# Kernel tuning notes

Measured on AMD Instinct MI355X. Metric: run time of the kernel, lower is better.

Reference implementation:

```python
import jax, jax.numpy as jnp
import numpy as np

N = 500_000            # nodes
E = 16_000_000         # used edges (var edges); E_total = 2*E
EPS = 1e-5             # BatchNorm eps
SQRT_C = np.sqrt(2.0).astype(np.float32)  # out_channels=2


def setup_inputs() -> dict:
    key = jax.random.key(0)
    ks = jax.random.split(key, 20)
    w = lambda k, s: (jax.random.normal(k, s, jnp.float32) * 0.5)
    d = {}
    d["x"] = jax.random.normal(ks[0], (N, 2), jnp.float32)
    d["edge_index"] = jax.random.randint(ks[1], (2, 2 * E), 0, N, jnp.int32)
    d["edge_attr"] = jax.random.normal(ks[2], (2 * E, 2), jnp.float32)
    d["mask"] = (jax.random.uniform(ks[3], (N,)) < 0.5).astype(jnp.float32)
    # TransformerConv(2,2,edge_dim=2,heads=1) params
    d["Wq"], d["bq"] = w(ks[4], (2, 2)), w(ks[5], (2,))
    d["Wk"], d["bk"] = w(ks[6], (2, 2)), w(ks[7], (2,))
    d["Wv"], d["bv"] = w(ks[8], (2, 2)), w(ks[9], (2,))
    d["We"] = w(ks[10], (2, 2))               # lin_edge, bias=False
    d["Wskip"], d["bskip"] = w(ks[11], (2, 2)), w(ks[12], (2,))
    # BatchNorm(2) affine params
    d["gamma"], d["beta"] = jnp.ones((2,), jnp.float32), jnp.zeros((2,), jnp.float32)
    # final Linear(2,1)
    d["Wf"], d["bf"] = w(ks[13], (1, 2)), w(ks[14], (1,))
    return d


def _transformer_conv(x, src, dst, ea, Wq, bq, Wk, bk, Wv, bv, We, Wskip, bskip):
    # PyG TransformerConv, heads=1, concat=True, root_weight=True, beta=False
    q = x @ Wq.T + bq                       # [N,2]
    k = x @ Wk.T + bk                       # [N,2]
    v = x @ Wv.T + bv                       # [N,2]
    e = ea @ We.T                           # [E,2]
    k_j = k[src] + e                        # [E,2]
    alpha = jnp.sum(q[dst] * k_j, axis=1) / SQRT_C  # [E]
    # segment softmax over destination nodes
    m = jax.ops.segment_max(alpha, dst, num_segments=N)          # -inf for empty
    m = jnp.where(jnp.isfinite(m), m, 0.0)
    a = jnp.exp(alpha - m[dst])
    s = jax.ops.segment_sum(a, dst, num_segments=N)
    wgt = a / jnp.where(s[dst] > 0, s[dst], 1.0)                 # [E]
    msg = (v[src] + e) * wgt[:, None]                            # [E,2]
    out = jax.ops.segment_sum(msg, dst, num_segments=N)          # [N,2]
    return out + x @ Wskip.T + bskip


def _neighbor_max(x, src, dst, ea_clause):
    # vectorized form of the per-node Python loop (scatter-max)
    s = jnp.sum(x[src] * ea_clause, axis=1)                      # [E]
    seg = jax.ops.segment_max(s, dst, num_segments=N)            # [N]
    deg = jax.ops.segment_sum(jnp.ones_like(s), dst, num_segments=N)
    has = deg > 0
    mx = jnp.where(has, seg, 0.0)
    stacked = jnp.stack([mx, 1.0 - mx], axis=1)                  # [N,2]
    return jnp.where(has[:, None], stacked, x)


def reference(x, edge_index, edge_attr, mask, Wq, bq, Wk, bk, Wv, bv, We,
              Wskip, bskip, gamma, beta, Wf, bf):
    ei = edge_index[:, 1::2]        # var_index = odd columns
    ea = edge_attr[1::2]            # var edge attrs
    ea_clause = edge_attr[0::2]     # clause edge attrs
    src, dst = ei[0], ei[1]
    h = _transformer_conv(x, src, dst, ea, Wq, bq, Wk, bk, Wv, bv, We, Wskip, bskip)
    # BatchNorm1d, training-mode batch statistics (biased var)
    mu = jnp.mean(h, axis=0)
    var = jnp.mean((h - mu) ** 2, axis=0)
    h = (h - mu) / jnp.sqrt(var + EPS) * gamma + beta
    # softmax over node dim (dim=0)
    h = jax.nn.softmax(h, axis=0)
    h = _neighbor_max(h, src, dst, ea_clause)
    # iterations=1 -> extra loop body does not execute
    out = jnp.squeeze(h @ Wf.T + bf)       # [N]
    return out * mask
```

## Files before the change

kernel.cpp:

```cpp
#include <hip/hip_runtime.h>
#include <hip/hip_fp16.h>

#define NNODES 500000
#define NEDGES 16000000
#define NBLK 1024
#define EPB (NEDGES / NBLK)
#define BSH 11
#define BSZ 2048
#define NBKT 245
#define BDIM 256
#define CHUNK 2048
#define KPC (CHUNK / 256)
#define CTH 1024

typedef unsigned long long u64;
typedef unsigned int u32;
typedef unsigned short u16;
typedef float vf4 __attribute__((ext_vector_type(4)));


__device__ __forceinline__ u32 fmap_ord(float x) {
    u32 u = __float_as_uint(x);
    return (u & 0x80000000u) ? ~u : (u | 0x80000000u);
}
__device__ __forceinline__ float funmap_ord(u32 u) {
    u32 bits = (u & 0x80000000u) ? (u ^ 0x80000000u) : ~u;
    return __uint_as_float(bits);
}

__device__ __forceinline__ float4 ntload4(const float4* p) {
    vf4 v = __builtin_nontemporal_load((const vf4*)p);
    return make_float4(v.x, v.y, v.z, v.w);
}

__device__ __forceinline__ void block_reduce_atomic4(float v0, float v1, float v2, float v3,
                                                     float* dst) {
    for (int off = 32; off > 0; off >>= 1) {
        v0 += __shfl_down(v0, off, 64);
        v1 += __shfl_down(v1, off, 64);
        v2 += __shfl_down(v2, off, 64);
        v3 += __shfl_down(v3, off, 64);
    }
    __shared__ float red[4][4];
    int lane = threadIdx.x & 63, wid = threadIdx.x >> 6;
    if (lane == 0) { red[wid][0] = v0; red[wid][1] = v1; red[wid][2] = v2; red[wid][3] = v3; }
    __syncthreads();
    if (threadIdx.x < 4) {
        float t = red[0][threadIdx.x] + red[1][threadIdx.x] + red[2][threadIdx.x] + red[3][threadIdx.x];
        unsafeAtomicAdd(&dst[threadIdx.x], t);
    }
}

__device__ __forceinline__ void block_reduce_atomic4_w16(float v0, float v1, float v2, float v3,
                                                         float* dst) {
    for (int off = 32; off > 0; off >>= 1) {
        v0 += __shfl_down(v0, off, 64);
        v1 += __shfl_down(v1, off, 64);
        v2 += __shfl_down(v2, off, 64);
        v3 += __shfl_down(v3, off, 64);
    }
    __shared__ float red[16][4];
    int lane = threadIdx.x & 63, wid = threadIdx.x >> 6;
    if (lane == 0) { red[wid][0] = v0; red[wid][1] = v1; red[wid][2] = v2; red[wid][3] = v3; }
    __syncthreads();
    if (threadIdx.x < 4) {
        float t = 0.f;
        #pragma unroll
        for (int w = 0; w < 16; ++w) t += red[w][threadIdx.x];
        unsafeAtomicAdd(&dst[threadIdx.x], t);
    }
}


__global__ __launch_bounds__(64) void k_zero_accum(float* accum) {
    if (threadIdx.x < 16) accum[threadIdx.x] = 0.f;
}

__global__ __launch_bounds__(256) void k_node_prep(
    const float* __restrict__ x,
    const float* __restrict__ Wq, const float* __restrict__ bq,
    const float* __restrict__ Wk, const float* __restrict__ bk,
    const float* __restrict__ Wv, const float* __restrict__ bv,
    float2* __restrict__ q, uint2* __restrict__ kvh) {
    int i = blockIdx.x * blockDim.x + threadIdx.x;
    if (i >= NNODES) return;
    float2 xv = ((const float2*)x)[i];
    float q0 = fmaf(Wq[0], xv.x, fmaf(Wq[1], xv.y, bq[0]));
    float q1 = fmaf(Wq[2], xv.x, fmaf(Wq[3], xv.y, bq[1]));
    float k0 = fmaf(Wk[0], xv.x, fmaf(Wk[1], xv.y, bk[0]));
    float k1 = fmaf(Wk[2], xv.x, fmaf(Wk[3], xv.y, bk[1]));
    float v0 = fmaf(Wv[0], xv.x, fmaf(Wv[1], xv.y, bv[0]));
    float v1 = fmaf(Wv[2], xv.x, fmaf(Wv[3], xv.y, bv[1]));
    q[i] = make_float2(q0, q1);
    __half2 hk = __floats2half2_rn(k0, k1);
    __half2 hv = __floats2half2_rn(v0, v1);
    kvh[i] = make_uint2(*(u32*)&hk, *(u32*)&hv);
}

__global__ void k_ln_final(const float* __restrict__ gamma, const float* __restrict__ beta,
                           float* __restrict__ accum) {
    float n = (float)NNODES;
    float mu0 = accum[0] / n, mu1 = accum[1] / n;
    float var0 = accum[2] / n - mu0 * mu0;
    float var1 = accum[3] / n - mu1 * mu1;
    float sc0 = gamma[0] * rsqrtf(var0 + 1e-5f);
    float sc1 = gamma[1] * rsqrtf(var1 + 1e-5f);
    accum[8] = sc0;
    accum[9] = sc1;
    accum[10] = beta[0] - mu0 * sc0;
    accum[11] = beta[1] - mu1 * sc1;
}

__global__ __launch_bounds__(256) void k_softmax(
    const float2* __restrict__ h, float2* __restrict__ pp, float* __restrict__ accum) {
    int i = blockIdx.x * blockDim.x + threadIdx.x;
    float p0 = 0.f, p1 = 0.f;
    if (i < NNODES) {
        float sc0 = accum[8], sc1 = accum[9], sh0 = accum[10], sh1 = accum[11];
        float2 hv = h[i];
        p0 = __expf(fmaf(hv.x, sc0, sh0));
        p1 = __expf(fmaf(hv.y, sc1, sh1));
        pp[i] = make_float2(p0, p1);
    }
    block_reduce_atomic4(p0, p1, 0.f, 0.f, accum + 4);
}

__global__ void k_sm_final(float* __restrict__ accum) {
    accum[12] = 1.f / accum[4];
    accum[13] = 1.f / accum[5];
}


__global__ __launch_bounds__(256) void k_hist(const int2* __restrict__ dst2, u32* __restrict__ M) {
    __shared__ u32 hist[BDIM];
    if (threadIdx.x < BDIM) hist[threadIdx.x] = 0u;
    __syncthreads();
    int beg = blockIdx.x * EPB, end = beg + EPB;
    #pragma unroll 4
    for (int e = beg + threadIdx.x; e < end; e += 256)
        atomicAdd(&hist[dst2[e].y >> BSH], 1u);
    __syncthreads();
    u32* row = M + (size_t)blockIdx.x * BDIM;
    if (threadIdx.x < BDIM) row[threadIdx.x] = hist[threadIdx.x];
}

__global__ __launch_bounds__(256) void k_bucket_prefix(u32* __restrict__ M, u32* __restrict__ bucketTotal) {
    __shared__ u32 col[NBLK];
    int b = blockIdx.x;
    for (int j = threadIdx.x; j < NBLK; j += 256) col[j] = M[(size_t)j * BDIM + b];
    __syncthreads();
    if (threadIdx.x == 0) {
        u32 run = 0;
        for (int j = 0; j < NBLK; ++j) { u32 c = col[j]; col[j] = run; run += c; }
        bucketTotal[b] = run;
    }
    __syncthreads();
    for (int j = threadIdx.x; j < NBLK; j += 256) M[(size_t)j * BDIM + b] = col[j];
}

__global__ __launch_bounds__(256) void k_scan_serial(const u32* __restrict__ bucketTotal,
                                                     u32* __restrict__ bucketBase) {
    __shared__ u32 t[BDIM];
    __shared__ u32 o[BDIM + 1];
    if (threadIdx.x < BDIM) t[threadIdx.x] = bucketTotal[threadIdx.x];
    __syncthreads();
    if (threadIdx.x == 0) {
        u32 run = 0;
        for (int j = 0; j < BDIM; ++j) { o[j] = run; run += t[j]; }
        o[BDIM] = run;
    }
    __syncthreads();
    for (int j = threadIdx.x; j < BDIM + 1; j += 256) bucketBase[j] = o[j];
}


__global__ __launch_bounds__(256) void k_scatter_stg(
    const int2* __restrict__ src2, const int2* __restrict__ dst2,
    const float4* __restrict__ ea4, const float* __restrict__ We,
    const u32* __restrict__ M, const u32* __restrict__ bucketBase,
    float4* __restrict__ R) {
    __shared__ u32 hist[BDIM];
    __shared__ u32 lbase[BDIM];
    __shared__ u32 gcur[BDIM];
    __shared__ u32 wsum[4];
    __shared__ float4 buf[CHUNK];
    __shared__ u16 bkt[CHUNK];

    const u32* row = M + (size_t)blockIdx.x * BDIM;
    if (threadIdx.x < BDIM) gcur[threadIdx.x] = row[threadIdx.x] + bucketBase[threadIdx.x];
    float we00 = We[0], we01 = We[1], we10 = We[2], we11 = We[3];
    int beg = blockIdx.x * EPB;
    int lane = threadIdx.x & 63, wid = threadIdx.x >> 6;

    for (int c0 = 0; c0 < EPB; c0 += CHUNK) {
        int cn = min(CHUNK, EPB - c0);
        if (threadIdx.x < BDIM) hist[threadIdx.x] = 0u;
        __syncthreads();

        float4 recs[KPC]; u32 bks[KPC]; u32 rnk[KPC]; bool val[KPC];
        #pragma unroll
        for (int k = 0; k < KPC; ++k) {
            int tt = k * 256 + threadIdx.x;
            val[k] = tt < cn;
            if (val[k]) {
                int e = beg + c0 + tt;
                int si = src2[e].y;
                int di = dst2[e].y;
                float4 eav = ea4[e];
                float e0 = fmaf(we00, eav.z, we01 * eav.w);
                float e1 = fmaf(we10, eav.z, we11 * eav.w);
                __half2 hc = __floats2half2_rn(eav.x, eav.y);
                u32 b = (u32)di >> BSH;
                u32 idx = (u32)si | ((u32)(di & (BSZ - 1)) << 19);
                recs[k] = make_float4(__uint_as_float(idx), e0, e1,
                                      __uint_as_float(*(u32*)&hc));
                bks[k] = b;
                rnk[k] = atomicAdd(&hist[b], 1u);
            }
        }
        __syncthreads();

        u32 s = hist[threadIdx.x];
        u32 inc = s;
        #pragma unroll
        for (int d = 1; d < 64; d <<= 1) {
            u32 v = __shfl_up(inc, d, 64);
            if (lane >= d) inc += v;
        }
        if (lane == 63) wsum[wid] = inc;
        __syncthreads();
        u32 woff = 0;
        for (int w = 0; w < wid; ++w) woff += wsum[w];
        lbase[threadIdx.x] = woff + inc - s;
        __syncthreads();

        #pragma unroll
        for (int k = 0; k < KPC; ++k) {
            if (val[k]) {
                u32 p = lbase[bks[k]] + rnk[k];
                buf[p] = recs[k];
                bkt[p] = (u16)bks[k];
            }
        }
        __syncthreads();

        for (int j = threadIdx.x; j < cn; j += 256) {
            u32 b = bkt[j];
            R[(size_t)gcur[b] + (u32)j - lbase[b]] = buf[j];
        }
        __syncthreads();

        if (threadIdx.x < BDIM) gcur[threadIdx.x] += hist[threadIdx.x];
        __syncthreads();
    }
}

__global__ __launch_bounds__(CTH) void k_attn16(
    const float4* __restrict__ R,
    const u32* __restrict__ bucketBase, const u32* __restrict__ bucketTotal,
    const uint2* __restrict__ kvh, const float2* __restrict__ qp,
    const float* __restrict__ x,
    const float* __restrict__ Wskip, const float* __restrict__ bskip,
    float2* __restrict__ h, float* __restrict__ accum) {
    __shared__ float sA[BSZ], m0A[BSZ], m1A[BSZ];
    __shared__ float2 qT[BSZ];
    int b = blockIdx.x, base = b << BSH;
    for (int j = threadIdx.x; j < BSZ; j += CTH) {
        sA[j] = 0.f; m0A[j] = 0.f; m1A[j] = 0.f;
        int i = base + j;
        qT[j] = (i < NNODES) ? qp[i] : make_float2(0.f, 0.f);
    }
    __syncthreads();
    int beg = bucketBase[b], end = beg + bucketTotal[b];
    int idx = beg + threadIdx.x;
    for (; idx + 3 * CTH < end; idx += 4 * CTH) {
        float4 r[4];
        #pragma unroll
        for (int u = 0; u < 4; ++u) r[u] = ntload4(&R[idx + u * CTH]);
        int li[4]; uint2 kvv[4];
        #pragma unroll
        for (int u = 0; u < 4; ++u) {
            u32 rec = __float_as_uint(r[u].x);
            li[u] = rec >> 19;
            kvv[u] = kvh[rec & 0x7FFFFu];
        }
        #pragma unroll
        for (int u = 0; u < 4; ++u) {
            float2 kf = __half22float2(*(__half2*)&kvv[u].x);
            float2 vf = __half22float2(*(__half2*)&kvv[u].y);
            float2 qv = qT[li[u]];
            float alpha = fmaf(qv.x, kf.x + r[u].y, qv.y * (kf.y + r[u].z)) * 0.70710678118654752f;
            float a = __expf(alpha);
            atomicAdd(&sA[li[u]], a);
            atomicAdd(&m0A[li[u]], a * (vf.x + r[u].y));
            atomicAdd(&m1A[li[u]], a * (vf.y + r[u].z));
        }
    }
    for (; idx < end; idx += CTH) {
        float4 r = ntload4(&R[idx]);
        u32 rec = __float_as_uint(r.x);
        int li = rec >> 19;
        uint2 kvv = kvh[rec & 0x7FFFFu];
        float2 kf = __half22float2(*(__half2*)&kvv.x);
        float2 vf = __half22float2(*(__half2*)&kvv.y);
        float2 qv = qT[li];
        float alpha = fmaf(qv.x, kf.x + r.y, qv.y * (kf.y + r.z)) * 0.70710678118654752f;
        float a = __expf(alpha);
        atomicAdd(&sA[li], a);
        atomicAdd(&m0A[li], a * (vf.x + r.y));
        atomicAdd(&m1A[li], a * (vf.y + r.z));
    }
    __syncthreads();
    float r0 = 0.f, r1 = 0.f, r2 = 0.f, r3 = 0.f;
    float w00 = Wskip[0], w01 = Wskip[1], w10 = Wskip[2], w11 = Wskip[3];
    float c0 = bskip[0], c1 = bskip[1];
    for (int j = threadIdx.x; j < BSZ; j += CTH) {
        int i = base + j;
        if (i < NNODES) {
            float2 xv = ((const float2*)x)[i];
            float s = sA[j];
            float inv = s > 0.f ? 1.f / s : 0.f;
            float h0 = fmaf(m0A[j], inv, fmaf(w00, xv.x, fmaf(w01, xv.y, c0)));
            float h1 = fmaf(m1A[j], inv, fmaf(w10, xv.x, fmaf(w11, xv.y, c1)));
            h[i] = make_float2(h0, h1);
            r0 += h0; r1 += h1; r2 += h0 * h0; r3 += h1 * h1;
        }
    }
    block_reduce_atomic4_w16(r0, r1, r2, r3, accum);
}

__global__ __launch_bounds__(CTH) void k_nmax16(
    const float4* __restrict__ R,
    const u32* __restrict__ bucketBase, const u32* __restrict__ bucketTotal,
    const float2* __restrict__ pp, const float* __restrict__ accum,
    const float* __restrict__ Wf, const float* __restrict__ bf,
    const float* __restrict__ mask, float* __restrict__ out) {
    __shared__ u32 mxA[BSZ];
    __shared__ float maskT[BSZ];
    int b = blockIdx.x, base = b << BSH;
    for (int j = threadIdx.x; j < BSZ; j += CTH) {
        mxA[j] = 0u;
        int i = base + j;
        maskT[j] = (i < NNODES) ? mask[i] : 0.f;
    }
    __syncthreads();
    float inv0 = accum[12], inv1 = accum[13];
    int beg = bucketBase[b], end = beg + bucketTotal[b];
    int idx = beg + threadIdx.x;
    for (; idx + 3 * CTH < end; idx += 4 * CTH) {
        float4 r[4];
        #pragma unroll
        for (int u = 0; u < 4; ++u) r[u] = ntload4(&R[idx + u * CTH]);
        #pragma unroll
        for (int u = 0; u < 4; ++u) {
            u32 rec = __float_as_uint(r[u].x);
            int li = rec >> 19;
            if (maskT[li] == 0.f) continue;
            int si = rec & 0x7FFFFu;
            u32 hcbits = __float_as_uint(r[u].w);
            __half2 hc = *(__half2*)&hcbits;
            float2 cf = __half22float2(hc);
            float2 pv = pp[si];
            float sE = fmaf(pv.x * inv0, cf.x, pv.y * inv1 * cf.y);
            atomicMax(&mxA[li], fmap_ord(sE));
        }
    }
    for (; idx < end; idx += CTH) {
        float4 r = ntload4(&R[idx]);
        u32 rec = __float_as_uint(r.x);
        int li = rec >> 19;
        if (maskT[li] == 0.f) continue;
        int si = rec & 0x7FFFFu;
        u32 hcbits = __float_as_uint(r.w);
        __half2 hc = *(__half2*)&hcbits;
        float2 cf = __half22float2(hc);
        float2 pv = pp[si];
        float sE = fmaf(pv.x * inv0, cf.x, pv.y * inv1 * cf.y);
        atomicMax(&mxA[li], fmap_ord(sE));
    }
    __syncthreads();
    float wf0 = Wf[0], wf1 = Wf[1], bb = bf[0];
    for (int j = threadIdx.x; j < BSZ; j += CTH) {
        int i = base + j;
        if (i >= NNODES) continue;
        u32 m = mxA[j];
        float h0, h1;
        if (m != 0u) { float v = funmap_ord(m); h0 = v; h1 = 1.f - v; }
        else { float2 pv = pp[i]; h0 = pv.x * inv0; h1 = pv.y * inv1; }
        out[i] = fmaf(wf0, h0, fmaf(wf1, h1, bb)) * maskT[j];
    }
}


__global__ __launch_bounds__(256) void k_init_f(float* s, float* msg, u32* mxb, float* accum) {
    int i = blockIdx.x * blockDim.x + threadIdx.x;
    if (i < NNODES) { s[i] = 0.f; mxb[i] = 0u; }
    if (i < 2 * NNODES) msg[i] = 0.f;
    if (i < 16) accum[i] = 0.f;
}

__global__ __launch_bounds__(256) void k_node_prep_f(
    const float* __restrict__ x,
    const float* __restrict__ Wq, const float* __restrict__ bq,
    const float* __restrict__ Wk, const float* __restrict__ bk,
    const float* __restrict__ Wv, const float* __restrict__ bv,
    float2* __restrict__ q, float4* __restrict__ kv) {
    int i = blockIdx.x * blockDim.x + threadIdx.x;
    if (i >= NNODES) return;
    float2 xv = ((const float2*)x)[i];
    float q0 = fmaf(Wq[0], xv.x, fmaf(Wq[1], xv.y, bq[0]));
    float q1 = fmaf(Wq[2], xv.x, fmaf(Wq[3], xv.y, bq[1]));
    float k0 = fmaf(Wk[0], xv.x, fmaf(Wk[1], xv.y, bk[0]));
    float k1 = fmaf(Wk[2], xv.x, fmaf(Wk[3], xv.y, bk[1]));
    float v0 = fmaf(Wv[0], xv.x, fmaf(Wv[1], xv.y, bv[0]));
    float v1 = fmaf(Wv[2], xv.x, fmaf(Wv[3], xv.y, bv[1]));
    q[i] = make_float2(q0, q1);
    kv[i] = make_float4(k0, k1, v0, v1);
}

__global__ __launch_bounds__(256) void k_edge_attn_f(
    const int* __restrict__ ei, const float* __restrict__ ea,
    const float* __restrict__ We,
    const float2* __restrict__ q, const float4* __restrict__ kv,
    float* __restrict__ s, float* __restrict__ msg) {
    int e = blockIdx.x * blockDim.x + threadIdx.x;
    if (e >= NEDGES) return;
    float we00 = We[0], we01 = We[1], we10 = We[2], we11 = We[3];
    int si = ((const int2*)ei)[e].y;
    int di = ((const int2*)(ei + 2 * NEDGES))[e].y;
    float2 eav = ((const float2*)ea)[2 * e + 1];
    float4 kvv = kv[si];
    float2 qv = q[di];
    float e0 = fmaf(we00, eav.x, we01 * eav.y);
    float e1 = fmaf(we10, eav.x, we11 * eav.y);
    float alpha = fmaf(qv.x, kvv.x + e0, qv.y * (kvv.y + e1)) * 0.70710678118654752f;
    float a = __expf(alpha);
    unsafeAtomicAdd(&s[di], a);
    unsafeAtomicAdd(&msg[2 * di], a * (kvv.z + e0));
    unsafeAtomicAdd(&msg[2 * di + 1], a * (kvv.w + e1));
}

__global__ __launch_bounds__(256) void k_node_h_f(
    const float* __restrict__ x,
    const float* __restrict__ Wskip, const float* __restrict__ bskip,
    const float* __restrict__ s, float* __restrict__ msg, float* __restrict__ accum) {
    int i = blockIdx.x * blockDim.x + threadIdx.x;
    float h0 = 0.f, h1 = 0.f;
    if (i < NNODES) {
        float2 xv = ((const float2*)x)[i];
        float sk0 = fmaf(Wskip[0], xv.x, fmaf(Wskip[1], xv.y, bskip[0]));
        float sk1 = fmaf(Wskip[2], xv.x, fmaf(Wskip[3], xv.y, bskip[1]));
        float sv = s[i];
        float inv = sv > 0.f ? 1.f / sv : 0.f;
        h0 = fmaf(msg[2 * i], inv, sk0);
        h1 = fmaf(msg[2 * i + 1], inv, sk1);
        msg[2 * i] = h0;
        msg[2 * i + 1] = h1;
    }
    block_reduce_atomic4(h0, h1, h0 * h0, h1 * h1, accum);
}

__global__ __launch_bounds__(256) void k_edge_nmax_f(
    const int* __restrict__ ei, const float* __restrict__ ea,
    const float2* __restrict__ pp, const float* __restrict__ accum,
    u32* __restrict__ mxb) {
    int e = blockIdx.x * blockDim.x + threadIdx.x;
    if (e >= NEDGES) return;
    float inv0 = accum[12], inv1 = accum[13];
    int si = ((const int2*)ei)[e].y;
    int di = ((const int2*)(ei + 2 * NEDGES))[e].y;
    float2 c = ((const float2*)ea)[2 * e];
    float2 pv = pp[si];
    float sE = fmaf(pv.x * inv0, c.x, pv.y * inv1 * c.y);
    atomicMax(&mxb[di], fmap_ord(sE));
}

__global__ __launch_bounds__(256) void k_final_f(
    const u32* __restrict__ mxb, const float2* __restrict__ pp,
    const float* __restrict__ accum,
    const float* __restrict__ Wf, const float* __restrict__ bf,
    const float* __restrict__ mask, float* __restrict__ out) {
    int i = blockIdx.x * blockDim.x + threadIdx.x;
    if (i >= NNODES) return;
    u32 m = mxb[i];
    float h0, h1;
    if (m != 0u) {
        float v = funmap_ord(m);
        h0 = v;
        h1 = 1.f - v;
    } else {
        float2 pv = pp[i];
        h0 = pv.x * accum[12];
        h1 = pv.y * accum[13];
    }
    out[i] = fmaf(Wf[0], h0, fmaf(Wf[1], h1, bf[0])) * mask[i];
}


extern "C" void kernel_launch(void* const* d_in, const int* in_sizes, int n_in,
                              void* d_out, int out_size, void* d_ws, size_t ws_size,
                              hipStream_t stream) {
    const float* x     = (const float*)d_in[0];
    const int*   ei    = (const int*)d_in[1];
    const float* ea    = (const float*)d_in[2];
    const float* mask  = (const float*)d_in[3];
    const float* Wq    = (const float*)d_in[4];
    const float* bq    = (const float*)d_in[5];
    const float* Wk    = (const float*)d_in[6];
    const float* bk    = (const float*)d_in[7];
    const float* Wv    = (const float*)d_in[8];
    const float* bv    = (const float*)d_in[9];
    const float* We    = (const float*)d_in[10];
    const float* Wskip = (const float*)d_in[11];
    const float* bskip = (const float*)d_in[12];
    const float* gamma = (const float*)d_in[13];
    const float* beta  = (const float*)d_in[14];
    const float* Wf    = (const float*)d_in[15];
    const float* bf    = (const float*)d_in[16];
    float* out = (float*)d_out;

    const size_t N = NNODES;
    const size_t E = NEDGES;
    const int B = 256;
    const int gridN = (NNODES + B - 1) / B;

    const int2*   src2 = (const int2*)ei;
    const int2*   dst2 = (const int2*)(ei + 2 * NEDGES);
    const float4* ea4  = (const float4*)ea;

    size_t need16 = 8 * N
                  + 16 * E
                  + 8 * N
                  + 8 * N
                  + 8 * N
                  + 4 * (size_t)NBLK * BDIM
                  + 4 * BDIM
                  + 4 * (BDIM + 16)
                  + 64;

    if (ws_size >= need16) {
        char* base = (char*)d_ws;
        uint2*  kvh = (uint2*)base;                 base += 8 * N;
        float4* R  = (float4*)base;                 base += 16 * E;
        float2* q  = (float2*)base;                 base += 8 * N;
        float2* h  = (float2*)base;                 base += 8 * N;
        float2* p  = (float2*)base;                 base += 8 * N;
        u32*    M  = (u32*)base;                    base += 4 * (size_t)NBLK * BDIM;
        u32*    bT = (u32*)base;                    base += 4 * BDIM;
        u32*    bB = (u32*)base;                    base += 4 * (BDIM + 16);
        float*  accum = (float*)base;

        k_zero_accum<<<1, 64, 0, stream>>>(accum);
        k_node_prep<<<gridN, B, 0, stream>>>(x, Wq, bq, Wk, bk, Wv, bv, q, kvh);
        k_hist<<<NBLK, B, 0, stream>>>(dst2, M);
        k_bucket_prefix<<<BDIM, B, 0, stream>>>(M, bT);
        k_scan_serial<<<1, B, 0, stream>>>(bT, bB);
        k_scatter_stg<<<NBLK, B, 0, stream>>>(src2, dst2, ea4, We, M, bB, R);
        k_attn16<<<NBKT, CTH, 0, stream>>>(R, bB, bT, kvh, q, x, Wskip, bskip, h, accum);
        k_ln_final<<<1, 1, 0, stream>>>(gamma, beta, accum);
        k_softmax<<<gridN, B, 0, stream>>>(h, p, accum);
        k_sm_final<<<1, 1, 0, stream>>>(accum);
        k_nmax16<<<NBKT, CTH, 0, stream>>>(R, bB, bT, p, accum, Wf, bf, mask, out);
    } else {
        float*  q   = (float*)d_ws;
        float*  kvf = q + 2 * N;
        float*  s   = kvf + 4 * N;
        float*  msg = s + N;
        u32*    mxb = (u32*)(msg + 2 * N);
        float*  accum = (float*)(mxb + N);
        int grid2N = (int)((2 * N + B - 1) / B);
        int gridE  = (NEDGES + B - 1) / B;

        k_init_f<<<grid2N, B, 0, stream>>>(s, msg, mxb, accum);
        k_node_prep_f<<<gridN, B, 0, stream>>>(x, Wq, bq, Wk, bk, Wv, bv, (float2*)q, (float4*)kvf);
        k_edge_attn_f<<<gridE, B, 0, stream>>>(ei, ea, We, (const float2*)q, (const float4*)kvf, s, msg);
        k_node_h_f<<<gridN, B, 0, stream>>>(x, Wskip, bskip, s, msg, accum);
        k_ln_final<<<1, 1, 0, stream>>>(gamma, beta, accum);
        k_softmax<<<gridN, B, 0, stream>>>((const float2*)msg, (float2*)q, accum);
        k_sm_final<<<1, 1, 0, stream>>>(accum);
        k_edge_nmax_f<<<gridE, B, 0, stream>>>(ei, ea, (const float2*)q, accum, mxb);
        k_final_f<<<gridN, B, 0, stream>>>(mxb, (const float2*)q, accum, Wf, bf, mask, out);
    }
}
```

Measured before the change: 649.4 us.

## Split each dst bucket across two blocks with partial buffers and combine kernels

The attention and neighbor-max bucket kernels now launch two blocks per destination bucket, each handling half of the bucket's edges and writing partial sums or maxima to global buffers. New per-node kernels (k_node_h, k_final) merge the two halves and do the epilogue (skip connection, BN stats, final linear and mask). The aim is to fill more CUs, since there are only 245 buckets on a 256-CU device. The cost is extra global partial-buffer traffic, two more kernel launches, and twice the shared-memory init per bucket.

Result: slower. 693.4 us (+6.8%).

```diff
diff --git a/kernel.cpp b/kernel.cpp
--- a/kernel.cpp
+++ b/kernel.cpp
@@ -12,6 +12,7 @@
 #define CHUNK 2048
 #define KPC (CHUNK / 256)
 #define CTH 1024
+#define NP ((size_t)NBKT * BSZ)
 
 typedef unsigned long long u64;
 typedef unsigned int u32;
@@ -47,26 +48,6 @@
     __syncthreads();
     if (threadIdx.x < 4) {
         float t = red[0][threadIdx.x] + red[1][threadIdx.x] + red[2][threadIdx.x] + red[3][threadIdx.x];
-        unsafeAtomicAdd(&dst[threadIdx.x], t);
-    }
-}
-
-__device__ __forceinline__ void block_reduce_atomic4_w16(float v0, float v1, float v2, float v3,
-                                                         float* dst) {
-    for (int off = 32; off > 0; off >>= 1) {
-        v0 += __shfl_down(v0, off, 64);
-        v1 += __shfl_down(v1, off, 64);
-        v2 += __shfl_down(v2, off, 64);
-        v3 += __shfl_down(v3, off, 64);
-    }
-    __shared__ float red[16][4];
-    int lane = threadIdx.x & 63, wid = threadIdx.x >> 6;
-    if (lane == 0) { red[wid][0] = v0; red[wid][1] = v1; red[wid][2] = v2; red[wid][3] = v3; }
-    __syncthreads();
-    if (threadIdx.x < 4) {
-        float t = 0.f;
-        #pragma unroll
-        for (int w = 0; w < 16; ++w) t += red[w][threadIdx.x];
         unsafeAtomicAdd(&dst[threadIdx.x], t);
     }
 }
@@ -259,19 +240,23 @@
     const float4* __restrict__ R,
     const u32* __restrict__ bucketBase, const u32* __restrict__ bucketTotal,
     const uint2* __restrict__ kvh, const float2* __restrict__ qp,
-    const float* __restrict__ x,
-    const float* __restrict__ Wskip, const float* __restrict__ bskip,
-    float2* __restrict__ h, float* __restrict__ accum) {
+    float* __restrict__ pS, float* __restrict__ pM0, float* __restrict__ pM1) {
     __shared__ float sA[BSZ], m0A[BSZ], m1A[BSZ];
     __shared__ float2 qT[BSZ];
-    int b = blockIdx.x, base = b << BSH;
+    int blk = blockIdx.x;
+    int b = blk >> 1, half = blk & 1;
+    int base = b << BSH;
     for (int j = threadIdx.x; j < BSZ; j += CTH) {
         sA[j] = 0.f; m0A[j] = 0.f; m1A[j] = 0.f;
         int i = base + j;
         qT[j] = (i < NNODES) ? qp[i] : make_float2(0.f, 0.f);
     }
     __syncthreads();
-    int beg = bucketBase[b], end = beg + bucketTotal[b];
+    int len = bucketTotal[b];
+    int hlen = (len + 1) >> 1;
+    int beg = (int)bucketBase[b] + (half ? hlen : 0);
+    int cnt = half ? (len - hlen) : hlen;
+    int end = beg + cnt;
     int idx = beg + threadIdx.x;
     for (; idx + 3 * CTH < end; idx += 4 * CTH) {
         float4 r[4];
@@ -311,33 +296,46 @@
         atomicAdd(&m1A[li], a * (vf.y + r.z));
     }
     __syncthreads();
-    float r0 = 0.f, r1 = 0.f, r2 = 0.f, r3 = 0.f;
-    float w00 = Wskip[0], w01 = Wskip[1], w10 = Wskip[2], w11 = Wskip[3];
-    float c0 = bskip[0], c1 = bskip[1];
+    size_t off = (size_t)half * NP + (size_t)b * BSZ;
     for (int j = threadIdx.x; j < BSZ; j += CTH) {
-        int i = base + j;
-        if (i < NNODES) {
-            float2 xv = ((const float2*)x)[i];
-            float s = sA[j];
-            float inv = s > 0.f ? 1.f / s : 0.f;
-            float h0 = fmaf(m0A[j], inv, fmaf(w00, xv.x, fmaf(w01, xv.y, c0)));
-            float h1 = fmaf(m1A[j], inv, fmaf(w10, xv.x, fmaf(w11, xv.y, c1)));
-            h[i] = make_float2(h0, h1);
-            r0 += h0; r1 += h1; r2 += h0 * h0; r3 += h1 * h1;
-        }
-    }
-    block_reduce_atomic4_w16(r0, r1, r2, r3, accum);
+        pS[off + j]  = sA[j];
+        pM0[off + j] = m0A[j];
+        pM1[off + j] = m1A[j];
+    }
+}
+
+__global__ __launch_bounds__(256) void k_node_h(
+    const float* __restrict__ x,
+    const float* __restrict__ Wskip, const float* __restrict__ bskip,
+    const float* __restrict__ pS, const float* __restrict__ pM0, const float* __restrict__ pM1,
+    float2* __restrict__ h, float* __restrict__ accum) {
+    int i = blockIdx.x * blockDim.x + threadIdx.x;
+    float h0 = 0.f, h1 = 0.f;
+    if (i < NNODES) {
+        float s  = pS[i]  + pS[i + NP];
+        float m0 = pM0[i] + pM0[i + NP];
+        float m1 = pM1[i] + pM1[i + NP];
+        float2 xv = ((const float2*)x)[i];
+        float sk0 = fmaf(Wskip[0], xv.x, fmaf(Wskip[1], xv.y, bskip[0]));
+        float sk1 = fmaf(Wskip[2], xv.x, fmaf(Wskip[3], xv.y, bskip[1]));
+        float inv = s > 0.f ? 1.f / s : 0.f;
+        h0 = fmaf(m0, inv, sk0);
+        h1 = fmaf(m1, inv, sk1);
+        h[i] = make_float2(h0, h1);
+    }
+    block_reduce_atomic4(h0, h1, h0 * h0, h1 * h1, accum);
 }
 
 __global__ __launch_bounds__(CTH) void k_nmax16(
     const float4* __restrict__ R,
     const u32* __restrict__ bucketBase, const u32* __restrict__ bucketTotal,
     const float2* __restrict__ pp, const float* __restrict__ accum,
-    const float* __restrict__ Wf, const float* __restrict__ bf,
-    const float* __restrict__ mask, float* __restrict__ out) {
+    const float* __restrict__ mask, u32* __restrict__ pMx) {
     __shared__ u32 mxA[BSZ];
     __shared__ float maskT[BSZ];
-    int b = blockIdx.x, base = b << BSH;
+    int blk = blockIdx.x;
+    int b = blk >> 1, half = blk & 1;
+    int base = b << BSH;
     for (int j = threadIdx.x; j < BSZ; j += CTH) {
         mxA[j] = 0u;
         int i = base + j;
@@ -345,7 +343,11 @@
     }
     __syncthreads();
     float inv0 = accum[12], inv1 = accum[13];
-    int beg = bucketBase[b], end = beg + bucketTotal[b];
+    int len = bucketTotal[b];
+    int hlen = (len + 1) >> 1;
+    int beg = (int)bucketBase[b] + (half ? hlen : 0);
+    int cnt = half ? (len - hlen) : hlen;
+    int end = beg + cnt;
     int idx = beg + threadIdx.x;
     for (; idx + 3 * CTH < end; idx += 4 * CTH) {
         float4 r[4];
@@ -379,16 +381,29 @@
         atomicMax(&mxA[li], fmap_ord(sE));
     }
     __syncthreads();
-    float wf0 = Wf[0], wf1 = Wf[1], bb = bf[0];
-    for (int j = threadIdx.x; j < BSZ; j += CTH) {
-        int i = base + j;
-        if (i >= NNODES) continue;
-        u32 m = mxA[j];
-        float h0, h1;
-        if (m != 0u) { float v = funmap_ord(m); h0 = v; h1 = 1.f - v; }
-        else { float2 pv = pp[i]; h0 = pv.x * inv0; h1 = pv.y * inv1; }
-        out[i] = fmaf(wf0, h0, fmaf(wf1, h1, bb)) * maskT[j];
-    }
+    size_t off = (size_t)half * NP + (size_t)b * BSZ;
+    for (int j = threadIdx.x; j < BSZ; j += CTH) pMx[off + j] = mxA[j];
+}
+
+__global__ __launch_bounds__(256) void k_final(
+    const u32* __restrict__ pMx, const float2* __restrict__ pp,
+    const float* __restrict__ accum,
+    const float* __restrict__ Wf, const float* __restrict__ bf,
+    const float* __restrict__ mask, float* __restrict__ out) {
+    int i = blockIdx.x * blockDim.x + threadIdx.x;
+    if (i >= NNODES) return;
+    u32 m = max(pMx[i], pMx[i + NP]);
+    float h0, h1;
+    if (m != 0u) {
+        float v = funmap_ord(m);
+        h0 = v;
+        h1 = 1.f - v;
+    } else {
+        float2 pv = pp[i];
+        h0 = pv.x * accum[12];
+        h1 = pv.y * accum[13];
+    }
+    out[i] = fmaf(Wf[0], h0, fmaf(Wf[1], h1, bf[0])) * mask[i];
 }
 
 
@@ -533,6 +548,8 @@
                   + 8 * N
                   + 8 * N
                   + 8 * N
+                  + 4 * 2 * NP * 3
+                  + 4 * 2 * NP
                   + 4 * (size_t)NBLK * BDIM
                   + 4 * BDIM
                   + 4 * (BDIM + 16)
@@ -545,6 +562,10 @@
         float2* q  = (float2*)base;                 base += 8 * N;
         float2* h  = (float2*)base;                 base += 8 * N;
         float2* p  = (float2*)base;                 base += 8 * N;
+        float*  pS  = (float*)base;                 base += 4 * 2 * NP;
+        float*  pM0 = (float*)base;                 base += 4 * 2 * NP;
+        float*  pM1 = (float*)base;                 base += 4 * 2 * NP;
+        u32*    pMx = (u32*)base;                   base += 4 * 2 * NP;
         u32*    M  = (u32*)base;                    base += 4 * (size_t)NBLK * BDIM;
         u32*    bT = (u32*)base;                    base += 4 * BDIM;
         u32*    bB = (u32*)base;                    base += 4 * (BDIM + 16);
@@ -556,11 +577,13 @@
         k_bucket_prefix<<<BDIM, B, 0, stream>>>(M, bT);
         k_scan_serial<<<1, B, 0, stream>>>(bT, bB);
         k_scatter_stg<<<NBLK, B, 0, stream>>>(src2, dst2, ea4, We, M, bB, R);
-        k_attn16<<<NBKT, CTH, 0, stream>>>(R, bB, bT, kvh, q, x, Wskip, bskip, h, accum);
+        k_attn16<<<NBKT * 2, CTH, 0, stream>>>(R, bB, bT, kvh, q, pS, pM0, pM1);
+        k_node_h<<<gridN, B, 0, stream>>>(x, Wskip, bskip, pS, pM0, pM1, h, accum);
         k_ln_final<<<1, 1, 0, stream>>>(gamma, beta, accum);
         k_softmax<<<gridN, B, 0, stream>>>(h, p, accum);
         k_sm_final<<<1, 1, 0, stream>>>(accum);
-        k_nmax16<<<NBKT, CTH, 0, stream>>>(R, bB, bT, p, accum, Wf, bf, mask, out);
+        k_nmax16<<<NBKT * 2, CTH, 0, stream>>>(R, bB, bT, p, accum, mask, pMx);
+        k_final<<<gridN, B, 0, stream>>>(pMx, p, accum, Wf, bf, mask, out);
     } else {
         float*  q   = (float*)d_ws;
         float*  kvf = q + 2 * N;
```
